# Performance work log

Measured on AMD Instinct MI355X. Metric: run time of the kernel, lower is better.

Reference implementation:

```python
import jax, jax.numpy as jnp
import numpy as np

BS, SQ, DIM, N = 32, 4096, 3, 15  # feat = DIM*N = 45


def setup_inputs() -> dict:
    key = jax.random.key(0)
    ks = jax.random.split(key, 12)
    inp = {
        "q": jax.random.normal(ks[0], (BS, SQ, DIM * N), dtype=jnp.float32),
        "k": jax.random.normal(ks[1], (BS, SQ, DIM * N), dtype=jnp.float32),
        "v": jax.random.normal(ks[2], (BS, SQ, DIM * N), dtype=jnp.float32),
        "distances": jax.random.normal(ks[3], (BS, SQ, N, N), dtype=jnp.float32),
        "is_test": 0,
        # nn.Linear(3, 3) params (W: [out,in], b: [out]) for q/k/v projections
        "Wq": jax.random.normal(ks[4], (DIM, DIM), dtype=jnp.float32) * 0.5,
        "bq": jax.random.normal(ks[5], (DIM,), dtype=jnp.float32) * 0.1,
        "Wk": jax.random.normal(ks[6], (DIM, DIM), dtype=jnp.float32) * 0.5,
        "bk": jax.random.normal(ks[7], (DIM,), dtype=jnp.float32) * 0.1,
        "Wv": jax.random.normal(ks[8], (DIM, DIM), dtype=jnp.float32) * 0.5,
        "bv": jax.random.normal(ks[9], (DIM,), dtype=jnp.float32) * 0.1,
        # nn.Linear(45, 45) output projection
        "Wo": jax.random.normal(ks[10], (DIM * N, DIM * N), dtype=jnp.float32) * 0.15,
        "bo": jax.random.normal(ks[11], (DIM * N,), dtype=jnp.float32) * 0.1,
    }
    return inp


def reference(q, k, v, distances, Wq, bq, Wk, bk, Wv, bv, Wo, bo, is_test):
    bs, sq, feat = q.shape
    dim, n = 3, feat // 3  # dim=3 coords per point, n=15 points; d_k=1, h=3

    def proj(x, W, b):
        # (bs, sq, feat) -> (bs, sq, dim, n) -> transpose -> (bs, sq, n, dim)
        xr = jnp.transpose(x.reshape(bs, sq, dim, n), (0, 1, 3, 2))
        y = jnp.einsum('bsnd,ed->bsne', xr, W) + b  # Linear(3,3): x @ W.T + b
        # view (bs, sq, n, h=3, d_k=1) then transpose(2,3) -> (bs, sq, h, n, 1);
        # squeeze the trailing d_k=1 for efficiency.
        return jnp.transpose(y, (0, 1, 3, 2))  # (bs, sq, h=3, n)

    qh = proj(q, Wq, bq)
    kh = proj(k, Wk, bk)  # k,v sliced to q's seq len (same here)
    vh = proj(v, Wv, bv)

    # scores = |q @ k^T| / sqrt(d_k), d_k=1 so divisor is 1; second abs is a no-op
    scores = jnp.abs(jnp.einsum('bshn,bshm->bshnm', qh, kh))  # (bs,sq,3,n,n)
    # softmax over the FLATTENED n*n axis
    scores = jax.nn.softmax(scores.reshape(bs, sq, dim, n * n), axis=-1)
    scores = scores.reshape(bs, sq, dim, n, n)
    # distance bias broadcast over the 3 heads (repeat along dim 2)
    scores_b = scores + 2.0 * distances[:, :, None, :, :]
    # (bs,sq,3,n,n) @ (bs,sq,3,n,1) -> (bs,sq,3,n)
    out = jnp.einsum('bshnm,bshm->bshn', scores_b, vh)
    # transpose(2,3), squeeze d_k, reshape to (bs, sq, 45) [n-major layout]
    concat = jnp.transpose(out, (0, 1, 3, 2)).reshape(bs, sq, dim * n)
    output = concat @ Wo.T + bo
    # train path: attention_value = np.zeros(seq)
    att_val = jnp.zeros((sq,), dtype=output.dtype)
    return output, att_val
```

## Files before the change

kernel.cpp:

```cpp
#include <hip/hip_runtime.h>

#define NT 64
#define TOK 64

#define GL16(gp, lp) __builtin_amdgcn_global_load_lds( \
    (const __attribute__((address_space(1))) void*)(gp), \
    (__attribute__((address_space(3))) void*)(lp), 16, 0, 0)
#define GL4(gp, lp) __builtin_amdgcn_global_load_lds( \
    (const __attribute__((address_space(1))) void*)(gp), \
    (__attribute__((address_space(3))) void*)(lp), 4, 0, 0)
#define WAITVM(N) do { \
    asm volatile("s_waitcnt vmcnt(" #N ")" ::: "memory"); \
    __builtin_amdgcn_sched_barrier(0); \
} while (0)
#define WAITLG() do { \
    asm volatile("s_waitcnt lgkmcnt(0)" ::: "memory"); \
    __builtin_amdgcn_sched_barrier(0); \
} while (0)

#if defined(__has_builtin)
# if __has_builtin(__builtin_amdgcn_exp2f)
#  define EXP2F(x) __builtin_amdgcn_exp2f(x)
# else
#  define EXP2F(x) exp2f(x)
# endif
#else
# define EXP2F(x) exp2f(x)
#endif

__device__ __forceinline__ void stage45(const float* __restrict__ g, float* lds, int lane) {
    const float4* g4 = (const float4*)g;
    #pragma unroll
    for (int it = 0; it < 11; ++it)
        GL16(g4 + it * 64 + lane, lds + it * 256);
    if (lane < 16) GL16(g4 + 704 + lane, lds + 2816);
}

__device__ __forceinline__ void stage_row(const float* __restrict__ dr, float* slot,
                                          int off0, int j0) {
    int off = off0, j = j0;
    #pragma unroll
    for (int it = 0; it < 15; ++it) {
        GL4(dr + off, slot + it * 64);
        j += 4;
        bool w = (j >= 15);
        j -= w ? 15 : 0;
        off += w ? 1114 : 904;
    }
}

template <bool ABS>
__device__ __forceinline__ void projr(const float* row, const float w[9], const float bb[3],
                                      float dst[3][15]) {
    #pragma unroll
    for (int n = 0; n < 15; ++n) {
        float x0 = row[n], x1 = row[15 + n], x2 = row[30 + n];
        #pragma unroll
        for (int h = 0; h < 3; ++h) {
            float y = fmaf(x2, w[h*3+2], fmaf(x1, w[h*3+1], fmaf(x0, w[h*3+0], bb[h])));
            dst[h][n] = ABS ? fabsf(y) : y;
        }
    }
}

#define SLOTP(r) ((r) % 5 == 0 ? dring : (r) % 5 == 1 ? dring + 960 : buf + ((r) % 5 - 2) * 960)

#define PHASE(p, WN) do { \
    WAITVM(WN); \
    { const float* sl = SLOTP(p) + lane * 15; \
      _Pragma("unroll") \
      for (int jj = 0; jj < 15; ++jj) { \
        float dd = sl[jj]; \
        concat[(p)*3 + 0] = fmaf(dd, vv[0][jj], concat[(p)*3 + 0]); \
        concat[(p)*3 + 1] = fmaf(dd, vv[1][jj], concat[(p)*3 + 1]); \
        concat[(p)*3 + 2] = fmaf(dd, vv[2][jj], concat[(p)*3 + 2]); \
      } } \
    if ((p) <= 9) { WAITLG(); stage_row(dbase + ((p)+5)*15, SLOTP(p), off0, j0); } \
} while (0)

__global__ __launch_bounds__(NT, 2) void mha_spatial_kernel(
    const float* __restrict__ q, const float* __restrict__ k, const float* __restrict__ v,
    const float* __restrict__ dist,
    const float* __restrict__ Wq, const float* __restrict__ bq,
    const float* __restrict__ Wk, const float* __restrict__ bk,
    const float* __restrict__ Wv, const float* __restrict__ bv,
    const float* __restrict__ Wo, const float* __restrict__ bo,
    float* __restrict__ out)
{
    __shared__ __align__(16) float buf[2880];
    __shared__ __align__(16) float dring[1920];
    const int lane = threadIdx.x;
    const int base = blockIdx.x * TOK;

    const float LOG2E = 1.4426950408889634f;
    float wq[9], wk[9], wv[9], bqv[3], bkv[3], bvv[3];
    #pragma unroll
    for (int i = 0; i < 9; ++i) { wq[i] = Wq[i] * LOG2E; wk[i] = Wk[i]; wv[i] = Wv[i]; }
    #pragma unroll
    for (int i = 0; i < 3; ++i) { bqv[i] = bq[i] * LOG2E; bkv[i] = bk[i]; bvv[i] = bv[i]; }

    float a[3][15], b[3][15], vv[3][15];

    stage45(q + (size_t)base * 45, buf, lane);
    WAITVM(0);
    projr<true>(buf + lane * 45, wq, bqv, a);
    WAITLG();
    stage45(k + (size_t)base * 45, buf, lane);
    WAITVM(0);
    projr<true>(buf + lane * 45, wk, bkv, b);
    WAITLG();

    const float* dbase = dist + (size_t)base * 225;
    const int tok0 = lane / 15, j0 = lane - tok0 * 15;
    const int off0 = tok0 * 225 + j0;

    stage45(v + (size_t)base * 45, buf, lane);
    stage_row(dbase +  0, dring,       off0, j0);
    stage_row(dbase + 15, dring + 960, off0, j0);
    WAITVM(30);
    projr<false>(buf + lane * 45, wv, bvv, vv);
    WAITLG();
    stage_row(dbase + 30, buf,        off0, j0);
    stage_row(dbase + 45, buf +  960, off0, j0);
    stage_row(dbase + 60, buf + 1920, off0, j0);

    float concat[45];
    #pragma unroll
    for (int h = 0; h < 3; ++h) {
        float amax = a[h][0], bmax = b[h][0];
        #pragma unroll
        for (int n = 1; n < 15; ++n) { amax = fmaxf(amax, a[h][n]); bmax = fmaxf(bmax, b[h][n]); }
        const float mm2 = amax * bmax;
        float zp[4] = {0.f, 0.f, 0.f, 0.f};
        float pv[15];
        #pragma unroll
        for (int i = 0; i < 15; ++i) pv[i] = 0.f;
        #pragma unroll
        for (int i = 0; i < 15; ++i)
            #pragma unroll
            for (int j = 0; j < 15; ++j) {
                float t = EXP2F(fmaf(a[h][i], b[h][j], -mm2));
                zp[j & 3] += t;
                pv[i] = fmaf(t, vv[h][j], pv[i]);
            }
        const float rz = 1.f / ((zp[0] + zp[1]) + (zp[2] + zp[3]));
        #pragma unroll
        for (int i = 0; i < 15; ++i) concat[i*3 + h] = pv[i] * rz;
    }
    #pragma unroll
    for (int h = 0; h < 3; ++h)
        #pragma unroll
        for (int j = 0; j < 15; ++j) vv[h][j] *= 2.f;

    PHASE( 0, 60); PHASE( 1, 60); PHASE( 2, 60); PHASE( 3, 60);
    PHASE( 4, 60); PHASE( 5, 60); PHASE( 6, 60); PHASE( 7, 60);
    PHASE( 8, 60); PHASE( 9, 60); PHASE(10, 60); PHASE(11, 45);
    PHASE(12, 30); PHASE(13, 15); PHASE(14, 0);
    WAITLG();

    #pragma unroll 3
    for (int o = 0; o < 45; ++o) {
        float acc = bo[o];
        const float* wr = Wo + o * 45;
        #pragma unroll
        for (int cc = 0; cc < 45; ++cc) acc = fmaf(concat[cc], wr[cc], acc);
        buf[lane * 45 + o] = acc;
    }
    WAITLG();
    {
        float4* o4 = (float4*)(out + (size_t)base * 45);
        const float4* s4 = (const float4*)buf;
        #pragma unroll
        for (int it = 0; it < 11; ++it) o4[it * 64 + lane] = s4[it * 64 + lane];
        if (lane < 16) o4[704 + lane] = s4[704 + lane];
    }
}

extern "C" void kernel_launch(void* const* d_in, const int* in_sizes, int n_in,
                              void* d_out, int out_size, void* d_ws, size_t ws_size,
                              hipStream_t stream) {
    const float* q  = (const float*)d_in[0];
    const float* k  = (const float*)d_in[1];
    const float* v  = (const float*)d_in[2];
    const float* ds = (const float*)d_in[3];
    const float* Wq = (const float*)d_in[5];
    const float* bq = (const float*)d_in[6];
    const float* Wk = (const float*)d_in[7];
    const float* bk = (const float*)d_in[8];
    const float* Wv = (const float*)d_in[9];
    const float* bv = (const float*)d_in[10];
    const float* Wo = (const float*)d_in[11];
    const float* bo = (const float*)d_in[12];
    float* out = (float*)d_out;

    hipMemsetAsync(out + (size_t)32 * 4096 * 45, 0, 4096 * sizeof(float), stream);

    mha_spatial_kernel<<<dim3((32 * 4096) / TOK), dim3(NT), 0, stream>>>(
        q, k, v, ds, Wq, bq, Wk, bk, Wv, bv, Wo, bo, out);
}
```

Measured before the change: 57.89 us.

## Split block into two waves of 32 tokens each and drop softmax max-subtraction

Each 128-thread block now runs two wavefronts, and each wave handles 32 tokens. Only half the lanes in a wave do the per-token compute, while all lanes still issue the staged global-to-LDS loads. This cuts the per-wave serial compute chain and the LDS footprint per token, with the aim of more waves in flight for latency hiding, at the cost of leaving half of each wave idle. The softmax max-subtraction is also removed, saving the max reductions but risking exp overflow on large scores.

```diff
diff --git a/kernel.cpp b/kernel.cpp
--- a/kernel.cpp
+++ b/kernel.cpp
@@ -1,7 +1,7 @@
 #include <hip/hip_runtime.h>
 
-#define NT 64
-#define TOK 64
+#define NT 128
+#define TPW 32
 
 #define GL16(gp, lp) __builtin_amdgcn_global_load_lds( \
     (const __attribute__((address_space(1))) void*)(gp), \
@@ -31,22 +31,23 @@
 __device__ __forceinline__ void stage45(const float* __restrict__ g, float* lds, int lane) {
     const float4* g4 = (const float4*)g;
     #pragma unroll
-    for (int it = 0; it < 11; ++it)
+    for (int it = 0; it < 5; ++it)
         GL16(g4 + it * 64 + lane, lds + it * 256);
-    if (lane < 16) GL16(g4 + 704 + lane, lds + 2816);
+    if (lane < 40) GL16(g4 + 320 + lane, lds + 1280);
 }
 
 __device__ __forceinline__ void stage_row(const float* __restrict__ dr, float* slot,
-                                          int off0, int j0) {
+                                          int off0, int j0, int lane) {
     int off = off0, j = j0;
     #pragma unroll
-    for (int it = 0; it < 15; ++it) {
+    for (int it = 0; it < 7; ++it) {
         GL4(dr + off, slot + it * 64);
         j += 4;
         bool w = (j >= 15);
         j -= w ? 15 : 0;
         off += w ? 1114 : 904;
     }
+    if (lane < TPW) GL4(dr + off, slot + 448);
 }
 
 template <bool ABS>
@@ -63,11 +64,12 @@
     }
 }
 
-#define SLOTP(r) ((r) % 5 == 0 ? dring : (r) % 5 == 1 ? dring + 960 : buf + ((r) % 5 - 2) * 960)
+#define SLOTP(r) ((r) % 5 == 0 ? myD : (r) % 5 == 1 ? myD + 480 : myBuf + ((r) % 5 - 2) * 480)
 
 #define PHASE(p, WN) do { \
     WAITVM(WN); \
-    { const float* sl = SLOTP(p) + lane * 15; \
+    if (lane < TPW) { \
+      const float* sl = SLOTP(p) + lane * 15; \
       _Pragma("unroll") \
       for (int jj = 0; jj < 15; ++jj) { \
         float dd = sl[jj]; \
@@ -75,10 +77,10 @@
         concat[(p)*3 + 1] = fmaf(dd, vv[1][jj], concat[(p)*3 + 1]); \
         concat[(p)*3 + 2] = fmaf(dd, vv[2][jj], concat[(p)*3 + 2]); \
       } } \
-    if ((p) <= 9) { WAITLG(); stage_row(dbase + ((p)+5)*15, SLOTP(p), off0, j0); } \
+    if ((p) <= 9) { WAITLG(); stage_row(dbase + ((p)+5)*15, SLOTP(p), off0, j0, lane); } \
 } while (0)
 
-__global__ __launch_bounds__(NT, 2) void mha_spatial_kernel(
+__global__ __launch_bounds__(NT, 4) void mha_spatial_kernel(
     const float* __restrict__ q, const float* __restrict__ k, const float* __restrict__ v,
     const float* __restrict__ dist,
     const float* __restrict__ Wq, const float* __restrict__ bq,
@@ -87,10 +89,13 @@
     const float* __restrict__ Wo, const float* __restrict__ bo,
     float* __restrict__ out)
 {
-    __shared__ __align__(16) float buf[2880];
-    __shared__ __align__(16) float dring[1920];
-    const int lane = threadIdx.x;
-    const int base = blockIdx.x * TOK;
+    __shared__ __align__(16) float buf[4800];
+    const int tid  = threadIdx.x;
+    const int lane = tid & 63;
+    const int w    = tid >> 6;
+    const int tokbase = blockIdx.x * 64 + w * TPW;
+    float* myBuf = buf + w * 2400;
+    float* myD   = buf + w * 2400 + 1440;
 
     const float LOG2E = 1.4426950408889634f;
     float wq[9], wk[9], wv[9], bqv[3], bkv[3], bvv[3];
@@ -98,81 +103,82 @@
     for (int i = 0; i < 9; ++i) { wq[i] = Wq[i] * LOG2E; wk[i] = Wk[i]; wv[i] = Wv[i]; }
     #pragma unroll
     for (int i = 0; i < 3; ++i) { bqv[i] = bq[i] * LOG2E; bkv[i] = bk[i]; bvv[i] = bv[i]; }
+    WAITVM(0);
 
     float a[3][15], b[3][15], vv[3][15];
 
-    stage45(q + (size_t)base * 45, buf, lane);
+    stage45(q + (size_t)tokbase * 45, myBuf, lane);
     WAITVM(0);
-    projr<true>(buf + lane * 45, wq, bqv, a);
-    WAITLG();
-    stage45(k + (size_t)base * 45, buf, lane);
+    if (lane < TPW) projr<true>(myBuf + lane * 45, wq, bqv, a);
+    WAITLG();
+    stage45(k + (size_t)tokbase * 45, myBuf, lane);
     WAITVM(0);
-    projr<true>(buf + lane * 45, wk, bkv, b);
-    WAITLG();
-
-    const float* dbase = dist + (size_t)base * 225;
+    if (lane < TPW) projr<true>(myBuf + lane * 45, wk, bkv, b);
+    WAITLG();
+
+    const float* dbase = dist + (size_t)tokbase * 225;
     const int tok0 = lane / 15, j0 = lane - tok0 * 15;
     const int off0 = tok0 * 225 + j0;
 
-    stage45(v + (size_t)base * 45, buf, lane);
-    stage_row(dbase +  0, dring,       off0, j0);
-    stage_row(dbase + 15, dring + 960, off0, j0);
-    WAITVM(30);
-    projr<false>(buf + lane * 45, wv, bvv, vv);
-    WAITLG();
-    stage_row(dbase + 30, buf,        off0, j0);
-    stage_row(dbase + 45, buf +  960, off0, j0);
-    stage_row(dbase + 60, buf + 1920, off0, j0);
+    stage45(v + (size_t)tokbase * 45, myBuf, lane);
+    stage_row(dbase +  0, myD,       off0, j0, lane);
+    stage_row(dbase + 15, myD + 480, off0, j0, lane);
+    WAITVM(16);
+    if (lane < TPW) projr<false>(myBuf + lane * 45, wv, bvv, vv);
+    WAITLG();
+    stage_row(dbase + 30, myBuf,       off0, j0, lane);
+    stage_row(dbase + 45, myBuf + 480, off0, j0, lane);
+    stage_row(dbase + 60, myBuf + 960, off0, j0, lane);
 
     float concat[45];
-    #pragma unroll
-    for (int h = 0; h < 3; ++h) {
-        float amax = a[h][0], bmax = b[h][0];
-        #pragma unroll
-        for (int n = 1; n < 15; ++n) { amax = fmaxf(amax, a[h][n]); bmax = fmaxf(bmax, b[h][n]); }
-        const float mm2 = amax * bmax;
-        float zp[4] = {0.f, 0.f, 0.f, 0.f};
-        float pv[15];
-        #pragma unroll
-        for (int i = 0; i < 15; ++i) pv[i] = 0.f;
-        #pragma unroll
-        for (int i = 0; i < 15; ++i)
-            #pragma unroll
-            for (int j = 0; j < 15; ++j) {
-                float t = EXP2F(fmaf(a[h][i], b[h][j], -mm2));
-                zp[j & 3] += t;
-                pv[i] = fmaf(t, vv[h][j], pv[i]);
-            }
-        const float rz = 1.f / ((zp[0] + zp[1]) + (zp[2] + zp[3]));
-        #pragma unroll
-        for (int i = 0; i < 15; ++i) concat[i*3 + h] = pv[i] * rz;
-    }
-    #pragma unroll
-    for (int h = 0; h < 3; ++h)
-        #pragma unroll
-        for (int j = 0; j < 15; ++j) vv[h][j] *= 2.f;
-
-    PHASE( 0, 60); PHASE( 1, 60); PHASE( 2, 60); PHASE( 3, 60);
-    PHASE( 4, 60); PHASE( 5, 60); PHASE( 6, 60); PHASE( 7, 60);
-    PHASE( 8, 60); PHASE( 9, 60); PHASE(10, 60); PHASE(11, 45);
-    PHASE(12, 30); PHASE(13, 15); PHASE(14, 0);
-    WAITLG();
-
-    #pragma unroll 3
-    for (int o = 0; o < 45; ++o) {
-        float acc = bo[o];
-        const float* wr = Wo + o * 45;
-        #pragma unroll
-        for (int cc = 0; cc < 45; ++cc) acc = fmaf(concat[cc], wr[cc], acc);
-        buf[lane * 45 + o] = acc;
+    if (lane < TPW) {
+        #pragma unroll
+        for (int h = 0; h < 3; ++h) {
+            float zp[4] = {0.f, 0.f, 0.f, 0.f};
+            float pv[15];
+            #pragma unroll
+            for (int i = 0; i < 15; ++i) pv[i] = 0.f;
+            #pragma unroll
+            for (int i = 0; i < 15; ++i)
+                #pragma unroll
+                for (int j = 0; j < 15; ++j) {
+                    float t = EXP2F(a[h][i] * b[h][j]);
+                    zp[j & 3] += t;
+                    pv[i] = fmaf(t, vv[h][j], pv[i]);
+                }
+            const float rz = 1.f / ((zp[0] + zp[1]) + (zp[2] + zp[3]));
+            #pragma unroll
+            for (int i = 0; i < 15; ++i) concat[i*3 + h] = pv[i] * rz;
+        }
+        #pragma unroll
+        for (int h = 0; h < 3; ++h)
+            #pragma unroll
+            for (int j = 0; j < 15; ++j) vv[h][j] *= 2.f;
+    }
+
+    PHASE( 0, 32); PHASE( 1, 32); PHASE( 2, 32); PHASE( 3, 32);
+    PHASE( 4, 32); PHASE( 5, 32); PHASE( 6, 32); PHASE( 7, 32);
+    PHASE( 8, 32); PHASE( 9, 32); PHASE(10, 32); PHASE(11, 24);
+    PHASE(12, 16); PHASE(13, 8);  PHASE(14, 0);
+    WAITLG();
+
+    if (lane < TPW) {
+        #pragma unroll 3
+        for (int o = 0; o < 45; ++o) {
+            float acc = bo[o];
+            const float* wr = Wo + o * 45;
+            #pragma unroll
+            for (int cc = 0; cc < 45; ++cc) acc = fmaf(concat[cc], wr[cc], acc);
+            myBuf[lane * 45 + o] = acc;
+        }
     }
     WAITLG();
     {
-        float4* o4 = (float4*)(out + (size_t)base * 45);
-        const float4* s4 = (const float4*)buf;
-        #pragma unroll
-        for (int it = 0; it < 11; ++it) o4[it * 64 + lane] = s4[it * 64 + lane];
-        if (lane < 16) o4[704 + lane] = s4[704 + lane];
+        float4* o4 = (float4*)(out + (size_t)tokbase * 45);
+        const float4* s4 = (const float4*)myBuf;
+        #pragma unroll
+        for (int it = 0; it < 5; ++it) o4[it * 64 + lane] = s4[it * 64 + lane];
+        if (lane < 40) o4[320 + lane] = s4[320 + lane];
     }
 }
 
@@ -195,6 +201,6 @@
 
     hipMemsetAsync(out + (size_t)32 * 4096 * 45, 0, 4096 * sizeof(float), stream);
 
-    mha_spatial_kernel<<<dim3((32 * 4096) / TOK), dim3(NT), 0, stream>>>(
+    mha_spatial_kernel<<<dim3(2048), dim3(NT), 0, stream>>>(
         q, k, v, ds, Wq, bq, Wk, bk, Wv, bv, Wo, bo, out);
 }
```

New measurement: 169.3 us. +192.4%, slower.
